# Performance work log

Hardware: AMD Instinct MI355X
Metric: run time of the kernel (lower is better)

The kernel has to match this reference:

```python
import jax, jax.numpy as jnp
import numpy as np

NUM_SELECTS = 2
NOISE_EPS = 0.01
LOSS_COEF = 0.01
INV_SQRT2 = 0.7071067811865476


def _phi(z):
    # standard normal CDF
    return 0.5 * (1.0 + jax.lax.erf(z * INV_SQRT2))


def _cv_squared(v, eps=1e-10):
    # torch .var() uses unbiased estimator (ddof=1)
    return jnp.var(v, ddof=1) / (jnp.mean(v) ** 2 + eps)


def setup_inputs() -> dict:
    key = jax.random.key(0)
    ks = jax.random.split(key, 5)
    T, D, E = 8192, 4096, 16
    return {
        "x": jax.random.normal(ks[0], (T, D), jnp.float32),
        "gate_w1": jax.random.normal(ks[1], (E, D), jnp.float32) * 0.02,
        "gate_w2": jax.random.normal(ks[2], (E, E), jnp.float32) * 0.02,
        "noise_w": jax.random.normal(ks[3], (E, D), jnp.float32) * 0.02,
        "noise": jax.random.normal(ks[4], (T, E), jnp.float32),
    }


def reference(x, gate_w1, gate_w2, noise_w, noise):
    T = x.shape[0]
    # gate network: Linear -> tanh -> Linear (no biases)
    logits_gate = jnp.tanh(x @ gate_w1.T) @ gate_w2.T          # [T, E]
    noise_control = jax.nn.softplus(x @ noise_w.T) + NOISE_EPS  # [T, E]
    logits_noise = noise * noise_control                        # [T, E]
    logits = logits_gate + logits_noise

    # top (k+1) for load-balancing thresholds
    top_logits, top_indices = jax.lax.top_k(logits, NUM_SELECTS + 1)
    top_k_logits = top_logits[:, :NUM_SELECTS]
    top_k_indices = top_indices[:, :NUM_SELECTS]
    top_k_scores = jax.nn.softmax(top_k_logits, axis=1)

    # importance: scatter top-k scores back to [T, E]
    rows = jnp.arange(T)[:, None]
    scores_filtered = jnp.zeros_like(logits).at[rows, top_k_indices].set(top_k_scores)
    importance = scores_filtered.sum(0)  # [E]

    # load: prob each expert would be in the top-k under the noise model
    thr_in = top_logits[:, NUM_SELECTS][:, None]        # (k+1)-th largest
    thr_out = top_logits[:, NUM_SELECTS - 1][:, None]   # k-th largest
    is_in = logits_noise > thr_in
    prob_if_in = _phi((logits_gate - thr_in) / noise_control)
    prob_if_out = _phi((logits_gate - thr_out) / noise_control)
    load = jnp.where(is_in, prob_if_in, prob_if_out).sum(0)  # [E]

    gate_loss = (_cv_squared(importance) + _cv_squared(load)) * LOSS_COEF
    return top_k_indices, top_k_scores, gate_loss
```

## Files before the change

### kernel.cpp

```cpp
#include <hip/hip_runtime.h>
#include <math.h>

#define TT 8192
#define DD 4096

typedef float  f32x4  __attribute__((ext_vector_type(4)));
typedef short  bf16x8 __attribute__((ext_vector_type(8)));
typedef unsigned int u32;

__global__ __launch_bounds__(128)
void split_w(const float* __restrict__ gw1, const float* __restrict__ nw,
             u32* __restrict__ wfrag) {
  const int s = blockIdx.x;
  const int t = threadIdx.x;
  const int h = t >> 6, l = t & 63;
  const int e = h * 16 + (l & 15);
  const float* src = ((e < 16) ? (gw1 + (size_t)e * DD) : (nw + (size_t)(e - 16) * DD))
                     + s * 32 + ((l >> 4) << 3);
  float f[8];
  *(float4*)&f[0] = *(const float4*)src;
  *(float4*)&f[4] = *(const float4*)(src + 4);
  u32 u0[8], u1[8], u2[8];
#pragma unroll
  for (int i = 0; i < 8; ++i) {
    u0[i] = __float_as_uint(f[i]);
    const float r1 = f[i] - __uint_as_float(u0[i] & 0xFFFF0000u);
    u1[i] = __float_as_uint(r1);
    const float r2 = r1 - __uint_as_float(u1[i] & 0xFFFF0000u);
    u2[i] = __float_as_uint(r2);
  }
  const size_t base = ((size_t)s * 2 + h) * 256 + l * 4;
#define PK(U) make_uint4((U[0]>>16)|(U[1]&0xFFFF0000u), (U[2]>>16)|(U[3]&0xFFFF0000u), \
                         (U[4]>>16)|(U[5]&0xFFFF0000u), (U[6]>>16)|(U[7]&0xFFFF0000u))
  *(uint4*)(wfrag + base)                 = PK(u0);
  *(uint4*)(wfrag + base + 128 * 512)     = PK(u1);
  *(uint4*)(wfrag + base + 2 * 128 * 512) = PK(u2);
#undef PK
}

__global__ __launch_bounds__(512, 4)
void gate_mega(const float* __restrict__ x, const u32* __restrict__ wfrag,
               const float* __restrict__ noise, const float* __restrict__ gw2,
               float* __restrict__ out, float* __restrict__ part2) {
  __shared__ float red[8][512];
  __shared__ float sg2[256];
  const int t = threadIdx.x;
  const int w = t >> 6, l = t & 63;
  const int rt = blockIdx.x;
  if (t < 256) sg2[t] = gw2[t];

  const int r = l & 15, c = l >> 4;
  const float* xp = x + (size_t)(rt * 16 + r) * DD + w * 512 + (c << 3);
  const u32* wfl = wfrag + (size_t)l * 4 + (size_t)(w * 16) * 512;

  f32x4 ag0 = {0,0,0,0}, ag1 = ag0, ag2 = ag0, an0 = ag0, an1 = ag0, an2 = ag0;

#pragma unroll 2
  for (int sl = 0; sl < 16; ++sl) {
    float f[8];
    *(float4*)&f[0] = *(const float4*)(xp + sl * 32);
    *(float4*)&f[4] = *(const float4*)(xp + sl * 32 + 4);

    const u32* wb = wfl + (size_t)sl * 512;
    const bf16x8 bg0 = *(const bf16x8*)(wb);
    const bf16x8 bn0 = *(const bf16x8*)(wb + 256);
    const bf16x8 bg1 = *(const bf16x8*)(wb + 128 * 512);
    const bf16x8 bn1 = *(const bf16x8*)(wb + 128 * 512 + 256);
    const bf16x8 bg2 = *(const bf16x8*)(wb + 2 * 128 * 512);
    const bf16x8 bn2 = *(const bf16x8*)(wb + 2 * 128 * 512 + 256);

    u32 pk[12] __attribute__((aligned(16)));
#pragma unroll
    for (int p = 0; p < 4; ++p) {
      const u32  a  = __float_as_uint(f[2*p]);
      const float ra1 = f[2*p] - __uint_as_float(a & 0xFFFF0000u);
      const u32  a1 = __float_as_uint(ra1);
      const float ra2 = ra1 - __uint_as_float(a1 & 0xFFFF0000u);
      const u32  a2 = __float_as_uint(ra2);
      const u32  b  = __float_as_uint(f[2*p+1]);
      const float rb1 = f[2*p+1] - __uint_as_float(b & 0xFFFF0000u);
      const u32  b1 = __float_as_uint(rb1);
      const float rb2 = rb1 - __uint_as_float(b1 & 0xFFFF0000u);
      const u32  b2 = __float_as_uint(rb2);
      pk[p]     = (a  >> 16) | (b  & 0xFFFF0000u);
      pk[4 + p] = (a1 >> 16) | (b1 & 0xFFFF0000u);
      pk[8 + p] = (a2 >> 16) | (b2 & 0xFFFF0000u);
    }
    const bf16x8 a0 = *(const bf16x8*)&pk[0];
    const bf16x8 a1 = *(const bf16x8*)&pk[4];
    const bf16x8 a2 = *(const bf16x8*)&pk[8];

    ag0 = __builtin_amdgcn_mfma_f32_16x16x32_bf16(a0, bg0, ag0, 0, 0, 0);
    an0 = __builtin_amdgcn_mfma_f32_16x16x32_bf16(a0, bn0, an0, 0, 0, 0);
    ag1 = __builtin_amdgcn_mfma_f32_16x16x32_bf16(a0, bg1, ag1, 0, 0, 0);
    an1 = __builtin_amdgcn_mfma_f32_16x16x32_bf16(a0, bn1, an1, 0, 0, 0);
    ag2 = __builtin_amdgcn_mfma_f32_16x16x32_bf16(a1, bg0, ag2, 0, 0, 0);
    an2 = __builtin_amdgcn_mfma_f32_16x16x32_bf16(a1, bn0, an2, 0, 0, 0);
    ag0 = __builtin_amdgcn_mfma_f32_16x16x32_bf16(a0, bg2, ag0, 0, 0, 0);
    an0 = __builtin_amdgcn_mfma_f32_16x16x32_bf16(a0, bn2, an0, 0, 0, 0);
    ag1 = __builtin_amdgcn_mfma_f32_16x16x32_bf16(a1, bg1, ag1, 0, 0, 0);
    an1 = __builtin_amdgcn_mfma_f32_16x16x32_bf16(a1, bn1, an1, 0, 0, 0);
    ag2 = __builtin_amdgcn_mfma_f32_16x16x32_bf16(a2, bg0, ag2, 0, 0, 0);
    an2 = __builtin_amdgcn_mfma_f32_16x16x32_bf16(a2, bn0, an2, 0, 0, 0);
  }

  const f32x4 cg = ag0 + ag1 + ag2;
  const f32x4 cn = an0 + an1 + an2;
#pragma unroll
  for (int j = 0; j < 4; ++j) {
    red[w][r * 16 + (c * 4 + j)]        = cg[j];
    red[w][(16 + r) * 16 + (c * 4 + j)] = cn[j];
  }
  __syncthreads();
  {
    float s = red[0][t];
#pragma unroll
    for (int ww = 1; ww < 8; ++ww) s += red[ww][t];
    red[0][t] = s;
  }
  __syncthreads();

  if (t < 16) {
    const int row = rt * 16 + t;
    float dot[32];
#pragma unroll
    for (int e = 0; e < 32; ++e) dot[e] = red[0][e * 16 + t];
    float h[16];
#pragma unroll
    for (int e = 0; e < 16; ++e) h[e] = tanhf(dot[e]);
    float lg[16], nc[16], ln[16], lo[16];
#pragma unroll
    for (int j = 0; j < 16; ++j) {
      float s = 0.f;
#pragma unroll
      for (int e = 0; e < 16; ++e) s = fmaf(h[e], sg2[j * 16 + e], s);
      lg[j] = s;
      const float v = dot[16 + j];
      nc[j] = fmaxf(v, 0.f) + log1pf(expf(-fabsf(v))) + 0.01f;
      ln[j] = noise[(size_t)row * 16 + j] * nc[j];
      lo[j] = lg[j] + ln[j];
    }
    int i0 = 0; float m0 = lo[0];
#pragma unroll
    for (int j = 1; j < 16; ++j) if (lo[j] > m0) { m0 = lo[j]; i0 = j; }
    int i1 = -1; float m1 = -1e30f;
#pragma unroll
    for (int j = 0; j < 16; ++j) if (j != i0 && lo[j] > m1) { m1 = lo[j]; i1 = j; }
    float m2 = -1e30f;
#pragma unroll
    for (int j = 0; j < 16; ++j) if (j != i0 && j != i1 && lo[j] > m2) m2 = lo[j];

    const float e1 = expf(m1 - m0);
    const float s0 = 1.f / (1.f + e1);
    const float s1 = e1 / (1.f + e1);
    out[(size_t)row * 2]             = (float)i0;
    out[(size_t)row * 2 + 1]         = (float)i1;
    out[16384 + (size_t)row * 2]     = s0;
    out[16384 + (size_t)row * 2 + 1] = s1;

    float cacc[32];
#pragma unroll
    for (int j = 0; j < 16; ++j) {
      cacc[j] = (j == i0) ? s0 : ((j == i1) ? s1 : 0.f);
      const bool in = ln[j] > m2;
      const float thr = in ? m2 : m1;
      const float z = (lg[j] - thr) / nc[j];
      cacc[16 + j] = 0.5f * (1.f + erff(z * 0.70710678118654752f));
    }
#pragma unroll
    for (int off = 1; off < 16; off <<= 1) {
#pragma unroll
      for (int k = 0; k < 32; ++k) cacc[k] += __shfl_xor(cacc[k], off, 16);
    }
    float v0 = 0.f, v1 = 0.f;
#pragma unroll
    for (int k = 0; k < 16; ++k) if (t == k) { v0 = cacc[k]; v1 = cacc[16 + k]; }
    part2[(size_t)rt * 32 + t]      = v0;
    part2[(size_t)rt * 32 + 16 + t] = v1;
  }
}

__global__ __launch_bounds__(256)
void gate_loss_k(const float* __restrict__ part2, float* __restrict__ out) {
  __shared__ float sred[8][32];
  const int t = threadIdx.x;
  const int k = t & 31, s = t >> 5;
  float acc = 0.f;
#pragma unroll 8
  for (int i = 0; i < 64; ++i) acc += part2[(size_t)(s * 64 + i) * 32 + k];
  sred[s][k] = acc;
  __syncthreads();
  if (t == 0) {
    float res = 0.f;
    for (int g = 0; g < 2; ++g) {
      float vals[16];
      float mu = 0.f;
      for (int j = 0; j < 16; ++j) {
        float s2 = 0.f;
        for (int ss = 0; ss < 8; ++ss) s2 += sred[ss][g * 16 + j];
        vals[j] = s2;
        mu += s2;
      }
      mu *= (1.f / 16.f);
      float var = 0.f;
      for (int j = 0; j < 16; ++j) { const float d = vals[j] - mu; var += d * d; }
      var *= (1.f / 15.f);
      res += var / (mu * mu + 1e-10f);
    }
    out[32768] = res * 0.01f;
  }
}

extern "C" void kernel_launch(void* const* d_in, const int* in_sizes, int n_in,
                              void* d_out, int out_size, void* d_ws, size_t ws_size,
                              hipStream_t stream) {
  const float* x     = (const float*)d_in[0];
  const float* gw1   = (const float*)d_in[1];
  const float* gw2   = (const float*)d_in[2];
  const float* nw    = (const float*)d_in[3];
  const float* noise = (const float*)d_in[4];
  float* out   = (float*)d_out;
  u32*   wfrag = (u32*)d_ws;
  float* part2 = (float*)((char*)d_ws + (size_t)768 * 1024);
  split_w<<<128, 128, 0, stream>>>(gw1, nw, wfrag);
  gate_mega<<<512, 512, 0, stream>>>(x, wfrag, noise, gw2, out, part2);
  gate_loss_k<<<1, 256, 0, stream>>>(part2, out);
}
```

Baseline: 61.23 us.

## Prefetch x tiles into a 3-stage LDS ring via global_load_lds

Replaces direct per-iteration global loads of x with asynchronous global_load_lds copies into a per-wave triple-buffered LDS ring. Three slices are issued up front, and manual vmcnt/lgkmcnt waits keep up to two slices in flight while MFMAs run. The K loop is also fully unrolled. This is meant to hide global memory latency on the x stream. In exchange it adds about 48KB of LDS per block, which may cut how many blocks fit per CU. It also relies on hand-counted vmcnt values staying correct alongside the compiler's own weight loads.

After: 63.07 us. 3.0% more time.

```diff
diff --git a/kernel.cpp b/kernel.cpp
--- a/kernel.cpp
+++ b/kernel.cpp
@@ -7,6 +7,10 @@
 typedef float  f32x4  __attribute__((ext_vector_type(4)));
 typedef short  bf16x8 __attribute__((ext_vector_type(8)));
 typedef unsigned int u32;
+
+typedef __attribute__((address_space(3))) void        lds_vp;
+typedef const __attribute__((address_space(1))) void  gbl_vp;
+#define GLD(gp_, lp_) __builtin_amdgcn_global_load_lds((gbl_vp*)(gp_), (lds_vp*)(lp_), 16, 0, 0)
 
 __global__ __launch_bounds__(128)
 void split_w(const float* __restrict__ gw1, const float* __restrict__ nw,
@@ -42,6 +46,7 @@
 void gate_mega(const float* __restrict__ x, const u32* __restrict__ wfrag,
                const float* __restrict__ noise, const float* __restrict__ gw2,
                float* __restrict__ out, float* __restrict__ part2) {
+  __shared__ __align__(16) float lds_x[8][3][512];
   __shared__ float red[8][512];
   __shared__ float sg2[256];
   const int t = threadIdx.x;
@@ -50,16 +55,27 @@
   if (t < 256) sg2[t] = gw2[t];
 
   const int r = l & 15, c = l >> 4;
-  const float* xp = x + (size_t)(rt * 16 + r) * DD + w * 512 + (c << 3);
+  const float* gx = x + (size_t)(rt * 16 + r) * DD + w * 512 + (c << 3);
   const u32* wfl = wfrag + (size_t)l * 4 + (size_t)(w * 16) * 512;
 
   f32x4 ag0 = {0,0,0,0}, ag1 = ag0, ag2 = ag0, an0 = ag0, an1 = ag0, an2 = ag0;
 
-#pragma unroll 2
+  GLD(gx + 0 * 32,     &lds_x[w][0][0]);
+  GLD(gx + 0 * 32 + 4, &lds_x[w][0][256]);
+  GLD(gx + 1 * 32,     &lds_x[w][1][0]);
+  GLD(gx + 1 * 32 + 4, &lds_x[w][1][256]);
+  GLD(gx + 2 * 32,     &lds_x[w][2][0]);
+  GLD(gx + 2 * 32 + 4, &lds_x[w][2][256]);
+
+#pragma unroll
   for (int sl = 0; sl < 16; ++sl) {
-    float f[8];
-    *(float4*)&f[0] = *(const float4*)(xp + sl * 32);
-    *(float4*)&f[4] = *(const float4*)(xp + sl * 32 + 4);
+    if (sl <= 13)      asm volatile("s_waitcnt vmcnt(4)" ::: "memory");
+    else if (sl == 14) asm volatile("s_waitcnt vmcnt(2)" ::: "memory");
+    else               asm volatile("s_waitcnt vmcnt(0)" ::: "memory");
+
+    const float* xb = &lds_x[w][sl % 3][0];
+    const f32x4 q0 = *(const f32x4*)(xb + (l << 2));
+    const f32x4 q1 = *(const f32x4*)(xb + 256 + (l << 2));
 
     const u32* wb = wfl + (size_t)sl * 512;
     const bf16x8 bg0 = *(const bf16x8*)(wb);
@@ -72,13 +88,15 @@
     u32 pk[12] __attribute__((aligned(16)));
 #pragma unroll
     for (int p = 0; p < 4; ++p) {
-      const u32  a  = __float_as_uint(f[2*p]);
-      const float ra1 = f[2*p] - __uint_as_float(a & 0xFFFF0000u);
+      const float fa = (p < 2 ? q0 : q1)[(p & 1) * 2];
+      const float fb = (p < 2 ? q0 : q1)[(p & 1) * 2 + 1];
+      const u32  a  = __float_as_uint(fa);
+      const float ra1 = fa - __uint_as_float(a & 0xFFFF0000u);
       const u32  a1 = __float_as_uint(ra1);
       const float ra2 = ra1 - __uint_as_float(a1 & 0xFFFF0000u);
       const u32  a2 = __float_as_uint(ra2);
-      const u32  b  = __float_as_uint(f[2*p+1]);
-      const float rb1 = f[2*p+1] - __uint_as_float(b & 0xFFFF0000u);
+      const u32  b  = __float_as_uint(fb);
+      const float rb1 = fb - __uint_as_float(b & 0xFFFF0000u);
       const u32  b1 = __float_as_uint(rb1);
       const float rb2 = rb1 - __uint_as_float(b1 & 0xFFFF0000u);
       const u32  b2 = __float_as_uint(rb2);
@@ -89,6 +107,12 @@
     const bf16x8 a0 = *(const bf16x8*)&pk[0];
     const bf16x8 a1 = *(const bf16x8*)&pk[4];
     const bf16x8 a2 = *(const bf16x8*)&pk[8];
+
+    asm volatile("s_waitcnt lgkmcnt(0)" ::: "memory");
+    if (sl + 3 < 16) {
+      GLD(gx + (sl + 3) * 32,     &lds_x[w][sl % 3][0]);
+      GLD(gx + (sl + 3) * 32 + 4, &lds_x[w][sl % 3][256]);
+    }
 
     ag0 = __builtin_amdgcn_mfma_f32_16x16x32_bf16(a0, bg0, ag0, 0, 0, 0);
     an0 = __builtin_amdgcn_mfma_f32_16x16x32_bf16(a0, bn0, an0, 0, 0, 0);
```

## Stage weight fragments in LDS via async loads, share across two row tiles

Applied to the files above, without the earlier changes.

Each block now covers 32 rows with 1024 threads, two groups of 8 waves, instead of 16 rows with 512 threads. The bf16-split weight fragments are loaded into double-buffered LDS with global_load_lds and shared by both row groups. Before, every wave fetched its weights straight from global memory. This halves weight traffic per row and overlaps the next slice's weight load with the current MFMAs. The cost is a block-wide barrier on every slice, a larger LDS footprint, and half as many blocks (256), which may hurt occupancy.

Result: no change. 61.21 us (-0.0%).

```diff
diff --git a/kernel.cpp b/kernel.cpp
--- a/kernel.cpp
+++ b/kernel.cpp
@@ -7,6 +7,10 @@
 typedef float  f32x4  __attribute__((ext_vector_type(4)));
 typedef short  bf16x8 __attribute__((ext_vector_type(8)));
 typedef unsigned int u32;
+
+typedef __attribute__((address_space(3))) void        lds_vp;
+typedef const __attribute__((address_space(1))) void  gbl_vp;
+#define GLD(gp_, lp_) __builtin_amdgcn_global_load_lds((gbl_vp*)(gp_), (lds_vp*)(lp_), 16, 0, 0)
 
 __global__ __launch_bounds__(128)
 void split_w(const float* __restrict__ gw1, const float* __restrict__ nw,
@@ -38,47 +42,73 @@
 #undef PK
 }
 
-__global__ __launch_bounds__(512, 4)
+__global__ __launch_bounds__(1024, 4)
 void gate_mega(const float* __restrict__ x, const u32* __restrict__ wfrag,
                const float* __restrict__ noise, const float* __restrict__ gw2,
                float* __restrict__ out, float* __restrict__ part2) {
-  __shared__ float red[8][512];
+  __shared__ __align__(16) u32 ldsb[2][8][6][256];
+  __shared__ float red[8][1024];
   __shared__ float sg2[256];
   const int t = threadIdx.x;
-  const int w = t >> 6, l = t & 63;
+  const int v = t >> 6, l = t & 63;
+  const int w = v & 7;
+  const int m = v >> 3;
   const int rt = blockIdx.x;
   if (t < 256) sg2[t] = gw2[t];
 
   const int r = l & 15, c = l >> 4;
-  const float* xp = x + (size_t)(rt * 16 + r) * DD + w * 512 + (c << 3);
-  const u32* wfl = wfrag + (size_t)l * 4 + (size_t)(w * 16) * 512;
+  const float* xp = x + (size_t)(rt * 32 + m * 16 + r) * DD + w * 512 + (c << 3);
+
+  const u32* srcb[3];
+  u32* dst0[3];
+  u32* dst1[3];
+#pragma unroll
+  for (int i = 0; i < 3; ++i) {
+    const int q = 3 * v + i, s = q / 6, p = q % 6;
+    srcb[i] = wfrag + (size_t)(p >> 1) * 65536 + (p & 1) * 256
+                    + (size_t)s * 16 * 512 + (l << 2);
+    dst0[i] = &ldsb[0][s][p][0];
+    dst1[i] = &ldsb[1][s][p][0];
+  }
+
+#pragma unroll
+  for (int i = 0; i < 3; ++i) GLD(srcb[i], dst0[i]);
+  asm volatile("s_waitcnt vmcnt(0)" ::: "memory");
+  asm volatile("s_barrier" ::: "memory");
 
   f32x4 ag0 = {0,0,0,0}, ag1 = ag0, ag2 = ag0, an0 = ag0, an1 = ag0, an2 = ag0;
 
 #pragma unroll 2
   for (int sl = 0; sl < 16; ++sl) {
+    if (sl + 1 < 16) {
+#pragma unroll
+      for (int i = 0; i < 3; ++i)
+        GLD(srcb[i] + (size_t)(sl + 1) * 512, (sl & 1) ? dst0[i] : dst1[i]);
+    }
+
+    const u32* wb = &ldsb[sl & 1][w][0][0] + (l << 2);
+    const bf16x8 bg0 = *(const bf16x8*)(wb);
+    const bf16x8 bn0 = *(const bf16x8*)(wb + 256);
+    const bf16x8 bg1 = *(const bf16x8*)(wb + 512);
+    const bf16x8 bn1 = *(const bf16x8*)(wb + 768);
+    const bf16x8 bg2 = *(const bf16x8*)(wb + 1024);
+    const bf16x8 bn2 = *(const bf16x8*)(wb + 1280);
+
     float f[8];
     *(float4*)&f[0] = *(const float4*)(xp + sl * 32);
     *(float4*)&f[4] = *(const float4*)(xp + sl * 32 + 4);
 
-    const u32* wb = wfl + (size_t)sl * 512;
-    const bf16x8 bg0 = *(const bf16x8*)(wb);
-    const bf16x8 bn0 = *(const bf16x8*)(wb + 256);
-    const bf16x8 bg1 = *(const bf16x8*)(wb + 128 * 512);
-    const bf16x8 bn1 = *(const bf16x8*)(wb + 128 * 512 + 256);
-    const bf16x8 bg2 = *(const bf16x8*)(wb + 2 * 128 * 512);
-    const bf16x8 bn2 = *(const bf16x8*)(wb + 2 * 128 * 512 + 256);
-
     u32 pk[12] __attribute__((aligned(16)));
 #pragma unroll
     for (int p = 0; p < 4; ++p) {
-      const u32  a  = __float_as_uint(f[2*p]);
-      const float ra1 = f[2*p] - __uint_as_float(a & 0xFFFF0000u);
+      const float fa = f[2 * p], fb = f[2 * p + 1];
+      const u32  a  = __float_as_uint(fa);
+      const float ra1 = fa - __uint_as_float(a & 0xFFFF0000u);
       const u32  a1 = __float_as_uint(ra1);
       const float ra2 = ra1 - __uint_as_float(a1 & 0xFFFF0000u);
       const u32  a2 = __float_as_uint(ra2);
-      const u32  b  = __float_as_uint(f[2*p+1]);
-      const float rb1 = f[2*p+1] - __uint_as_float(b & 0xFFFF0000u);
+      const u32  b  = __float_as_uint(fb);
+      const float rb1 = fb - __uint_as_float(b & 0xFFFF0000u);
       const u32  b1 = __float_as_uint(rb1);
       const float rb2 = rb1 - __uint_as_float(b1 & 0xFFFF0000u);
       const u32  b2 = __float_as_uint(rb2);
@@ -102,14 +132,17 @@
     an1 = __builtin_amdgcn_mfma_f32_16x16x32_bf16(a1, bn1, an1, 0, 0, 0);
     ag2 = __builtin_amdgcn_mfma_f32_16x16x32_bf16(a2, bg0, ag2, 0, 0, 0);
     an2 = __builtin_amdgcn_mfma_f32_16x16x32_bf16(a2, bn0, an2, 0, 0, 0);
+
+    asm volatile("s_waitcnt vmcnt(0)" ::: "memory");
+    asm volatile("s_barrier" ::: "memory");
   }
 
   const f32x4 cg = ag0 + ag1 + ag2;
   const f32x4 cn = an0 + an1 + an2;
 #pragma unroll
   for (int j = 0; j < 4; ++j) {
-    red[w][r * 16 + (c * 4 + j)]        = cg[j];
-    red[w][(16 + r) * 16 + (c * 4 + j)] = cn[j];
+    red[w][m * 512 + r * 16 + (c * 4 + j)]        = cg[j];
+    red[w][m * 512 + (16 + r) * 16 + (c * 4 + j)] = cn[j];
   }
   __syncthreads();
   {
@@ -120,11 +153,12 @@
   }
   __syncthreads();
 
-  if (t < 16) {
-    const int row = rt * 16 + t;
+  if (t < 32) {
+    const int mg = t >> 4, rr = t & 15;
+    const int row = rt * 32 + t;
     float dot[32];
 #pragma unroll
-    for (int e = 0; e < 32; ++e) dot[e] = red[0][e * 16 + t];
+    for (int e = 0; e < 32; ++e) dot[e] = red[0][mg * 512 + e * 16 + rr];
     float h[16];
 #pragma unroll
     for (int e = 0; e < 16; ++e) h[e] = tanhf(dot[e]);
@@ -135,8 +169,8 @@
 #pragma unroll
       for (int e = 0; e < 16; ++e) s = fmaf(h[e], sg2[j * 16 + e], s);
       lg[j] = s;
-      const float v = dot[16 + j];
-      nc[j] = fmaxf(v, 0.f) + log1pf(expf(-fabsf(v))) + 0.01f;
+      const float vv = dot[16 + j];
+      nc[j] = fmaxf(vv, 0.f) + log1pf(expf(-fabsf(vv))) + 0.01f;
       ln[j] = noise[(size_t)row * 16 + j] * nc[j];
       lo[j] = lg[j] + ln[j];
     }
@@ -172,11 +206,12 @@
 #pragma unroll
       for (int k = 0; k < 32; ++k) cacc[k] += __shfl_xor(cacc[k], off, 16);
     }
+    const int g = rt * 2 + mg;
     float v0 = 0.f, v1 = 0.f;
 #pragma unroll
-    for (int k = 0; k < 16; ++k) if (t == k) { v0 = cacc[k]; v1 = cacc[16 + k]; }
-    part2[(size_t)rt * 32 + t]      = v0;
-    part2[(size_t)rt * 32 + 16 + t] = v1;
+    for (int k = 0; k < 16; ++k) if (rr == k) { v0 = cacc[k]; v1 = cacc[16 + k]; }
+    part2[(size_t)g * 32 + rr]      = v0;
+    part2[(size_t)g * 32 + 16 + rr] = v1;
   }
 }
 
@@ -223,6 +258,6 @@
   u32*   wfrag = (u32*)d_ws;
   float* part2 = (float*)((char*)d_ws + (size_t)768 * 1024);
   split_w<<<128, 128, 0, stream>>>(gw1, nw, wfrag);
-  gate_mega<<<512, 512, 0, stream>>>(x, wfrag, noise, gw2, out, part2);
+  gate_mega<<<256, 1024, 0, stream>>>(x, wfrag, noise, gw2, out, part2);
   gate_loss_k<<<1, 256, 0, stream>>>(part2, out);
 }
```

## Process 32 rows per block to reuse weight fragments across two row tiles

Applied to the files above, without the earlier changes.

Each block of the fused gate kernel now handles two 16-row tiles of x, so every loaded weight fragment feeds twice as many MFMAs and total weight-fragment traffic is halved. The grid shrinks from 512 to 256 blocks, and the LDS reduction buffer and epilogue are widened to 32 rows. The cost is double the accumulator registers and half as many blocks, which may cut occupancy or leave CUs idle on a 256-CU part. Partial sums for the loss are still written per 16-row group, so the final reduction kernel is unchanged.

After: 60.23 us, median of 2. Within noise of the previous version (-1.6%).

```diff
diff --git a/kernel.cpp b/kernel.cpp
--- a/kernel.cpp
+++ b/kernel.cpp
@@ -42,7 +42,7 @@
 void gate_mega(const float* __restrict__ x, const u32* __restrict__ wfrag,
                const float* __restrict__ noise, const float* __restrict__ gw2,
                float* __restrict__ out, float* __restrict__ part2) {
-  __shared__ float red[8][512];
+  __shared__ float red[8][1024];
   __shared__ float sg2[256];
   const int t = threadIdx.x;
   const int w = t >> 6, l = t & 63;
@@ -50,17 +50,36 @@
   if (t < 256) sg2[t] = gw2[t];
 
   const int r = l & 15, c = l >> 4;
-  const float* xp = x + (size_t)(rt * 16 + r) * DD + w * 512 + (c << 3);
+  const float* xp0 = x + (size_t)(rt * 32 + r) * DD + w * 512 + (c << 3);
+  const float* xp1 = xp0 + (size_t)16 * DD;
   const u32* wfl = wfrag + (size_t)l * 4 + (size_t)(w * 16) * 512;
 
-  f32x4 ag0 = {0,0,0,0}, ag1 = ag0, ag2 = ag0, an0 = ag0, an1 = ag0, an2 = ag0;
+  f32x4 g00 = {0,0,0,0}, g01 = g00, g02 = g00, n00 = g00, n01 = g00, n02 = g00;
+  f32x4 g10 = g00, g11 = g00, g12 = g00, n10 = g00, n11 = g00, n12 = g00;
+
+#define SPLIT8(FP, A0, A1, A2) \
+  u32 pk_[12] __attribute__((aligned(16))); \
+  { _Pragma("unroll") for (int p = 0; p < 4; ++p) { \
+      const float fa = FP[2*p], fb = FP[2*p+1]; \
+      const u32  a  = __float_as_uint(fa); \
+      const float ra1 = fa - __uint_as_float(a & 0xFFFF0000u); \
+      const u32  a1 = __float_as_uint(ra1); \
+      const float ra2 = ra1 - __uint_as_float(a1 & 0xFFFF0000u); \
+      const u32  a2 = __float_as_uint(ra2); \
+      const u32  b  = __float_as_uint(fb); \
+      const float rb1 = fb - __uint_as_float(b & 0xFFFF0000u); \
+      const u32  b1 = __float_as_uint(rb1); \
+      const float rb2 = rb1 - __uint_as_float(b1 & 0xFFFF0000u); \
+      const u32  b2 = __float_as_uint(rb2); \
+      pk_[p]     = (a  >> 16) | (b  & 0xFFFF0000u); \
+      pk_[4 + p] = (a1 >> 16) | (b1 & 0xFFFF0000u); \
+      pk_[8 + p] = (a2 >> 16) | (b2 & 0xFFFF0000u); } } \
+  const bf16x8 A0 = *(const bf16x8*)&pk_[0]; \
+  const bf16x8 A1 = *(const bf16x8*)&pk_[4]; \
+  const bf16x8 A2 = *(const bf16x8*)&pk_[8];
 
 #pragma unroll 2
   for (int sl = 0; sl < 16; ++sl) {
-    float f[8];
-    *(float4*)&f[0] = *(const float4*)(xp + sl * 32);
-    *(float4*)&f[4] = *(const float4*)(xp + sl * 32 + 4);
-
     const u32* wb = wfl + (size_t)sl * 512;
     const bf16x8 bg0 = *(const bf16x8*)(wb);
     const bf16x8 bn0 = *(const bf16x8*)(wb + 256);
@@ -69,62 +88,71 @@
     const bf16x8 bg2 = *(const bf16x8*)(wb + 2 * 128 * 512);
     const bf16x8 bn2 = *(const bf16x8*)(wb + 2 * 128 * 512 + 256);
 
-    u32 pk[12] __attribute__((aligned(16)));
-#pragma unroll
-    for (int p = 0; p < 4; ++p) {
-      const u32  a  = __float_as_uint(f[2*p]);
-      const float ra1 = f[2*p] - __uint_as_float(a & 0xFFFF0000u);
-      const u32  a1 = __float_as_uint(ra1);
-      const float ra2 = ra1 - __uint_as_float(a1 & 0xFFFF0000u);
-      const u32  a2 = __float_as_uint(ra2);
-      const u32  b  = __float_as_uint(f[2*p+1]);
-      const float rb1 = f[2*p+1] - __uint_as_float(b & 0xFFFF0000u);
-      const u32  b1 = __float_as_uint(rb1);
-      const float rb2 = rb1 - __uint_as_float(b1 & 0xFFFF0000u);
-      const u32  b2 = __float_as_uint(rb2);
-      pk[p]     = (a  >> 16) | (b  & 0xFFFF0000u);
-      pk[4 + p] = (a1 >> 16) | (b1 & 0xFFFF0000u);
-      pk[8 + p] = (a2 >> 16) | (b2 & 0xFFFF0000u);
-    }
-    const bf16x8 a0 = *(const bf16x8*)&pk[0];
-    const bf16x8 a1 = *(const bf16x8*)&pk[4];
-    const bf16x8 a2 = *(const bf16x8*)&pk[8];
-
-    ag0 = __builtin_amdgcn_mfma_f32_16x16x32_bf16(a0, bg0, ag0, 0, 0, 0);
-    an0 = __builtin_amdgcn_mfma_f32_16x16x32_bf16(a0, bn0, an0, 0, 0, 0);
-    ag1 = __builtin_amdgcn_mfma_f32_16x16x32_bf16(a0, bg1, ag1, 0, 0, 0);
-    an1 = __builtin_amdgcn_mfma_f32_16x16x32_bf16(a0, bn1, an1, 0, 0, 0);
-    ag2 = __builtin_amdgcn_mfma_f32_16x16x32_bf16(a1, bg0, ag2, 0, 0, 0);
-    an2 = __builtin_amdgcn_mfma_f32_16x16x32_bf16(a1, bn0, an2, 0, 0, 0);
-    ag0 = __builtin_amdgcn_mfma_f32_16x16x32_bf16(a0, bg2, ag0, 0, 0, 0);
-    an0 = __builtin_amdgcn_mfma_f32_16x16x32_bf16(a0, bn2, an0, 0, 0, 0);
-    ag1 = __builtin_amdgcn_mfma_f32_16x16x32_bf16(a1, bg1, ag1, 0, 0, 0);
-    an1 = __builtin_amdgcn_mfma_f32_16x16x32_bf16(a1, bn1, an1, 0, 0, 0);
-    ag2 = __builtin_amdgcn_mfma_f32_16x16x32_bf16(a2, bg0, ag2, 0, 0, 0);
-    an2 = __builtin_amdgcn_mfma_f32_16x16x32_bf16(a2, bn0, an2, 0, 0, 0);
-  }
-
-  const f32x4 cg = ag0 + ag1 + ag2;
-  const f32x4 cn = an0 + an1 + an2;
+    {
+      float f[8];
+      *(float4*)&f[0] = *(const float4*)(xp0 + sl * 32);
+      *(float4*)&f[4] = *(const float4*)(xp0 + sl * 32 + 4);
+      SPLIT8(f, a0, a1, a2)
+      g00 = __builtin_amdgcn_mfma_f32_16x16x32_bf16(a0, bg0, g00, 0, 0, 0);
+      n00 = __builtin_amdgcn_mfma_f32_16x16x32_bf16(a0, bn0, n00, 0, 0, 0);
+      g01 = __builtin_amdgcn_mfma_f32_16x16x32_bf16(a0, bg1, g01, 0, 0, 0);
+      n01 = __builtin_amdgcn_mfma_f32_16x16x32_bf16(a0, bn1, n01, 0, 0, 0);
+      g02 = __builtin_amdgcn_mfma_f32_16x16x32_bf16(a1, bg0, g02, 0, 0, 0);
+      n02 = __builtin_amdgcn_mfma_f32_16x16x32_bf16(a1, bn0, n02, 0, 0, 0);
+      g00 = __builtin_amdgcn_mfma_f32_16x16x32_bf16(a0, bg2, g00, 0, 0, 0);
+      n00 = __builtin_amdgcn_mfma_f32_16x16x32_bf16(a0, bn2, n00, 0, 0, 0);
+      g01 = __builtin_amdgcn_mfma_f32_16x16x32_bf16(a1, bg1, g01, 0, 0, 0);
+      n01 = __builtin_amdgcn_mfma_f32_16x16x32_bf16(a1, bn1, n01, 0, 0, 0);
+      g02 = __builtin_amdgcn_mfma_f32_16x16x32_bf16(a2, bg0, g02, 0, 0, 0);
+      n02 = __builtin_amdgcn_mfma_f32_16x16x32_bf16(a2, bn0, n02, 0, 0, 0);
+    }
+    {
+      float f[8];
+      *(float4*)&f[0] = *(const float4*)(xp1 + sl * 32);
+      *(float4*)&f[4] = *(const float4*)(xp1 + sl * 32 + 4);
+      SPLIT8(f, a0, a1, a2)
+      g10 = __builtin_amdgcn_mfma_f32_16x16x32_bf16(a0, bg0, g10, 0, 0, 0);
+      n10 = __builtin_amdgcn_mfma_f32_16x16x32_bf16(a0, bn0, n10, 0, 0, 0);
+      g11 = __builtin_amdgcn_mfma_f32_16x16x32_bf16(a0, bg1, g11, 0, 0, 0);
+      n11 = __builtin_amdgcn_mfma_f32_16x16x32_bf16(a0, bn1, n11, 0, 0, 0);
+      g12 = __builtin_amdgcn_mfma_f32_16x16x32_bf16(a1, bg0, g12, 0, 0, 0);
+      n12 = __builtin_amdgcn_mfma_f32_16x16x32_bf16(a1, bn0, n12, 0, 0, 0);
+      g10 = __builtin_amdgcn_mfma_f32_16x16x32_bf16(a0, bg2, g10, 0, 0, 0);
+      n10 = __builtin_amdgcn_mfma_f32_16x16x32_bf16(a0, bn2, n10, 0, 0, 0);
+      g11 = __builtin_amdgcn_mfma_f32_16x16x32_bf16(a1, bg1, g11, 0, 0, 0);
+      n11 = __builtin_amdgcn_mfma_f32_16x16x32_bf16(a1, bn1, n11, 0, 0, 0);
+      g12 = __builtin_amdgcn_mfma_f32_16x16x32_bf16(a2, bg0, g12, 0, 0, 0);
+      n12 = __builtin_amdgcn_mfma_f32_16x16x32_bf16(a2, bn0, n12, 0, 0, 0);
+    }
+  }
+#undef SPLIT8
+
+  const f32x4 cg0 = g00 + g01 + g02;
+  const f32x4 cn0 = n00 + n01 + n02;
+  const f32x4 cg1 = g10 + g11 + g12;
+  const f32x4 cn1 = n10 + n11 + n12;
 #pragma unroll
   for (int j = 0; j < 4; ++j) {
-    red[w][r * 16 + (c * 4 + j)]        = cg[j];
-    red[w][(16 + r) * 16 + (c * 4 + j)] = cn[j];
+    red[w][r * 32 + (c * 4 + j)]             = cg0[j];
+    red[w][(16 + r) * 32 + (c * 4 + j)]      = cn0[j];
+    red[w][r * 32 + 16 + (c * 4 + j)]        = cg1[j];
+    red[w][(16 + r) * 32 + 16 + (c * 4 + j)] = cn1[j];
   }
   __syncthreads();
-  {
-    float s = red[0][t];
-#pragma unroll
-    for (int ww = 1; ww < 8; ++ww) s += red[ww][t];
-    red[0][t] = s;
+#pragma unroll
+  for (int idx = t; idx < 1024; idx += 512) {
+    float s = red[0][idx];
+#pragma unroll
+    for (int ww = 1; ww < 8; ++ww) s += red[ww][idx];
+    red[0][idx] = s;
   }
   __syncthreads();
 
-  if (t < 16) {
-    const int row = rt * 16 + t;
+  if (t < 32) {
+    const int row = rt * 32 + t;
     float dot[32];
 #pragma unroll
-    for (int e = 0; e < 32; ++e) dot[e] = red[0][e * 16 + t];
+    for (int e = 0; e < 32; ++e) dot[e] = red[0][e * 32 + t];
     float h[16];
 #pragma unroll
     for (int e = 0; e < 16; ++e) h[e] = tanhf(dot[e]);
@@ -172,11 +200,13 @@
 #pragma unroll
       for (int k = 0; k < 32; ++k) cacc[k] += __shfl_xor(cacc[k], off, 16);
     }
+    const int g = rt * 2 + (t >> 4);
+    const int rr = t & 15;
     float v0 = 0.f, v1 = 0.f;
 #pragma unroll
-    for (int k = 0; k < 16; ++k) if (t == k) { v0 = cacc[k]; v1 = cacc[16 + k]; }
-    part2[(size_t)rt * 32 + t]      = v0;
-    part2[(size_t)rt * 32 + 16 + t] = v1;
+    for (int k = 0; k < 16; ++k) if (rr == k) { v0 = cacc[k]; v1 = cacc[16 + k]; }
+    part2[(size_t)g * 32 + rr]      = v0;
+    part2[(size_t)g * 32 + 16 + rr] = v1;
   }
 }
 
@@ -223,6 +253,6 @@
   u32*   wfrag = (u32*)d_ws;
   float* part2 = (float*)((char*)d_ws + (size_t)768 * 1024);
   split_w<<<128, 128, 0, stream>>>(gw1, nw, wfrag);
-  gate_mega<<<512, 512, 0, stream>>>(x, wfrag, noise, gw2, out, part2);
+  gate_mega<<<256, 512, 0, stream>>>(x, wfrag, noise, gw2, out, part2);
   gate_loss_k<<<1, 256, 0, stream>>>(part2, out);
 }
```
